# Kernel tuning notes

Measured on AMD Instinct MI355X. Metric: run time of the kernel, lower is better.

Reference implementation:

```python
import jax, jax.numpy as jnp
import numpy as np

P = 7          # output_size
SR = 2         # sampling_ratio
SCALES = (0.25, 0.125, 0.0625, 0.03125)
K_MIN, K_MAX = 2.0, 5.0   # -log2(max scale), -log2(min scale)
LVL0, S0, EPS = 4.0, 224.0, 1e-6  # torchvision LevelMapper defaults


def _coverage(x1, x2, size):
    """Fractional per-pixel coverage of interval [x1, x2] along an axis.
    Reproduces fill_masks_for_boxes edge weighting. x1, x2: [K] -> [K, size]."""
    cols = jnp.arange(size, dtype=x1.dtype)[None, :]
    x1f = jnp.floor(x1)[:, None]
    x2c = jnp.ceil(x2)[:, None]
    inside = ((cols >= x1f) & (cols < x2c)).astype(x1.dtype)
    wl = jnp.where(cols == x1f, 1.0 + x1f - x1[:, None], 1.0)
    wr = jnp.where(cols == x2c - 1.0, 1.0 + x2[:, None] - x2c, 1.0)
    return inside * wl * wr


def _axis_interp(coord, size):
    """torchvision roi_align (aligned=False) 1D bilinear setup.
    Returns lo/hi indices and weights (zeroed for out-of-range points)."""
    valid = ((coord >= -1.0) & (coord <= size)).astype(coord.dtype)
    c = jnp.maximum(coord, 0.0)
    lo0 = jnp.floor(c)
    top = lo0 >= size - 1
    lo = jnp.where(top, float(size - 1), lo0)
    hi = jnp.where(top, float(size - 1), lo0 + 1.0)
    c = jnp.where(top, float(size - 1), c)
    frac = c - lo
    return lo.astype(jnp.int32), hi.astype(jnp.int32), (1.0 - frac) * valid, frac * valid


def _level_roi(feat, scale, ub, bo, bidx):
    """Masked RoIAlign of the union box over one pyramid level.
    feat: [N,C,H,W]; ub, bo: [K,4] image-coord boxes; bidx: [K] int32."""
    N, C, H, W = feat.shape
    K = ub.shape[0]
    ubs = ub * scale
    bos = bo * scale

    def clipb(b):
        return (jnp.clip(b[:, 0], 0.0, W), jnp.clip(b[:, 1], 0.0, H),
                jnp.clip(b[:, 2], 0.0, W), jnp.clip(b[:, 3], 0.0, H))

    ux1, uy1, ux2, uy2 = clipb(ubs)
    ox1, oy1, ox2, oy2 = clipb(bos)
    # Separable pair-mask coverage (NOTE: torch code mutates boxes_h into the
    # union in-place before mask construction, so the 'h' mask is the union mask).
    cxu = _coverage(ux1, ux2, W)  # [K,W]
    cyu = _coverage(uy1, uy2, H)  # [K,H]
    cxo = _coverage(ox1, ox2, W)
    cyo = _coverage(oy1, oy2, H)

    x1, y1, x2, y2 = ubs[:, 0], ubs[:, 1], ubs[:, 2], ubs[:, 3]
    roi_w = jnp.maximum(x2 - x1, 1.0)
    roi_h = jnp.maximum(y2 - y1, 1.0)
    i = jnp.arange(P * SR)
    t = (i // SR).astype(jnp.float32) + ((i % SR).astype(jnp.float32) + 0.5) / SR  # bin units
    px = x1[:, None] + t[None, :] * (roi_w / P)[:, None]  # [K, P*SR]
    py = y1[:, None] + t[None, :] * (roi_h / P)[:, None]
    xlo, xhi, wxl, wxh = _axis_interp(px, W)
    ylo, yhi, wyl, wyh = _axis_interp(py, H)

    ga = lambda tab, idx: jnp.take_along_axis(tab, idx, axis=1)
    ys, wy = (ylo, yhi), (wyl, wyh)
    xs, wx = (xlo, xhi), (wxl, wxh)
    myu = (ga(cyu, ylo), ga(cyu, yhi))
    mxu = (ga(cxu, xlo), ga(cxu, xhi))
    myo = (ga(cyo, ylo), ga(cyo, yhi))
    mxo = (ga(cxo, xlo), ga(cxo, xhi))

    acc = jnp.zeros((K, P * SR, P * SR, C), dtype=feat.dtype)
    for a in range(2):
        for b in range(2):
            # gather corner features: [K, Ps, Ps, C]
            fv = feat[bidx[:, None, None], :, ys[a][:, :, None], xs[b][:, None, :]]
            m = jnp.maximum(myu[a][:, :, None] * mxu[b][:, None, :],
                            myo[a][:, :, None] * mxo[b][:, None, :])
            wgt = wy[a][:, :, None] * wx[b][:, None, :] * m
            acc = acc + wgt[..., None] * fv
    out = acc.reshape(K, P, SR, P, SR, C).mean(axis=(2, 4))  # avg over sample grid
    return jnp.transpose(out, (0, 3, 1, 2))  # [K, C, P, P]


def _forward(feat0, feat1, feat2, feat3, boxes_h, boxes_o):
    feats = (feat0, feat1, feat2, feat3)
    bidx = boxes_h[:, 0].astype(jnp.int32)
    bh = boxes_h[:, 1:]
    bo = boxes_o[:, 1:]
    ub = jnp.stack([jnp.minimum(bh[:, 0], bo[:, 0]), jnp.minimum(bh[:, 1], bo[:, 1]),
                    jnp.maximum(bh[:, 2], bo[:, 2]), jnp.maximum(bh[:, 3], bo[:, 3])], axis=1)
    # Level mapping (boxes_h already mutated into the union in the torch code)
    su = jnp.sqrt((ub[:, 2] - ub[:, 0]) * (ub[:, 3] - ub[:, 1]))
    so = jnp.sqrt((bo[:, 2] - bo[:, 0]) * (bo[:, 3] - bo[:, 1]))
    s = jnp.minimum(su, so)
    lv = (jnp.clip(jnp.floor(LVL0 + jnp.log2(s / S0 + EPS)), K_MIN, K_MAX)).astype(jnp.int32) - int(K_MIN)
    K, C = boxes_h.shape[0], feat0.shape[1]
    out = jnp.zeros((K, C, P, P), dtype=feat0.dtype)
    for l, (f, sc) in enumerate(zip(feats, SCALES)):
        ol = _level_roi(f, sc, ub, bo, bidx)
        out = out + jnp.where((lv == l)[:, None, None, None], ol, 0.0)
    return out


def setup_inputs() -> dict:
    key = jax.random.key(0)
    ks = jax.random.split(key, 12)
    feat0 = jax.random.normal(ks[0], (2, 256, 128, 128), dtype=jnp.float32)
    feat1 = jax.random.normal(ks[1], (2, 256, 64, 64), dtype=jnp.float32)
    feat2 = jax.random.normal(ks[2], (2, 256, 32, 32), dtype=jnp.float32)
    feat3 = jax.random.normal(ks[3], (2, 256, 16, 16), dtype=jnp.float32)
    K = 512
    bidx = jax.random.randint(ks[4], (K,), 0, 2).astype(jnp.float32)

    def mk(k):
        k1, k2, k3, k4 = jax.random.split(k, 4)
        x1 = jax.random.uniform(k1, (K,), minval=0.0, maxval=112.0)
        y1 = jax.random.uniform(k2, (K,), minval=0.0, maxval=112.0)
        w = jax.random.uniform(k3, (K,), minval=16.0, maxval=400.0)
        h = jax.random.uniform(k4, (K,), minval=16.0, maxval=400.0)
        return jnp.stack([bidx, x1, y1, x1 + w, y1 + h], axis=1)  # image is 512x512

    return {"feat0": feat0, "feat1": feat1, "feat2": feat2, "feat3": feat3,
            "boxes_h": mk(ks[5]), "boxes_o": mk(ks[6])}


def reference(feat0, feat1, feat2, feat3, boxes_h, boxes_o):
    return _forward(feat0, feat1, feat2, feat3, boxes_h, boxes_o)
```

## Files before the change

### kernel.cpp

```cpp
#include <hip/hip_runtime.h>
#include <math.h>

#define PP 7
#define CCH 256

__device__ __forceinline__ float coverage(float colf, float a, float b) {
    float af = floorf(a);
    float bc = ceilf(b);
    float v  = (colf >= af && colf < bc) ? 1.0f : 0.0f;
    float wl = (colf == af) ? (1.0f + af - a) : 1.0f;
    float wr = (colf == bc - 1.0f) ? (1.0f + b - bc) : 1.0f;
    return v * wl * wr;
}

__global__ __launch_bounds__(256) void nchw_to_nhwc(const float* __restrict__ src,
                                                    float* __restrict__ dst, int HW)
{
    __shared__ float tile[64][65];
    const int tx = threadIdx.x & 63, ty = threadIdx.x >> 6;
    const int pix0 = blockIdx.x * 64;
    const int c0   = blockIdx.y * 64;
    const int n    = blockIdx.z;

    const float* s = src + ((size_t)n * CCH + c0) * HW + pix0;
    #pragma unroll
    for (int i = 0; i < 16; ++i) {
        const int r = i*4 + ty;
        tile[r][tx] = s[(size_t)r * HW + tx];
    }
    __syncthreads();
    float* d = dst + ((size_t)n * HW + pix0) * CCH + c0;
    #pragma unroll
    for (int i = 0; i < 16; ++i) {
        const int p = i*4 + ty;
        d[(size_t)p * CCH + tx] = tile[tx][p];
    }
}

__global__ __launch_bounds__(256) void roi_gather_nhwc(
    const float* __restrict__ n0, const float* __restrict__ n1,
    const float* __restrict__ n2, const float* __restrict__ n3,
    const float* __restrict__ bh, const float* __restrict__ bo,
    float* __restrict__ out, int K)
{
    const int k  = blockIdx.x;
    const int py = blockIdx.y;
    const int c  = threadIdx.x;

    __shared__ int   t_xoff_lo[14], t_xoff_hi[14];
    __shared__ float t_wxl[14], t_wxh[14];
    __shared__ float t_cxu0[14], t_cxu1[14], t_cxo0[14], t_cxo1[14];
    __shared__ int   s_yoff_lo[2], s_yoff_hi[2];
    __shared__ float s_wyl[2], s_wyh[2];
    __shared__ float s_cyu0[2], s_cyu1[2], s_cyo0[2], s_cyo1[2];

    const float hx1 = bh[k*5+1], hy1 = bh[k*5+2], hx2 = bh[k*5+3], hy2 = bh[k*5+4];
    const float px1 = bo[k*5+1], py1 = bo[k*5+2], px2 = bo[k*5+3], py2 = bo[k*5+4];
    const int   bimg = (int)bh[k*5+0];

    const float ux1 = fminf(hx1, px1), uy1 = fminf(hy1, py1);
    const float ux2 = fmaxf(hx2, px2), uy2 = fmaxf(hy2, py2);
    const float su = sqrtf((ux2-ux1)*(uy2-uy1));
    const float so = sqrtf((px2-px1)*(py2-py1));
    const float s  = fminf(su, so);
    float lvf = floorf(4.0f + log2f(s/224.0f + 1e-6f));
    lvf = fminf(fmaxf(lvf, 2.0f), 5.0f);
    const int lv = (int)lvf - 2;

    const float scales[4] = {0.25f, 0.125f, 0.0625f, 0.03125f};
    const int   dims[4]   = {128, 64, 32, 16};
    const float scale = scales[lv];
    const int   W = dims[lv], H = W;
    const int   HW = W * H;
    const float Wf = (float)W, Hf = (float)H;
    const float* nh = (lv == 0) ? n0 : (lv == 1) ? n1 : (lv == 2) ? n2 : n3;

    const float usx1 = ux1*scale, usy1 = uy1*scale, usx2 = ux2*scale, usy2 = uy2*scale;
    const float osx1 = px1*scale, osy1 = py1*scale, osx2 = px2*scale, osy2 = py2*scale;
    const float cux1 = fminf(fmaxf(usx1, 0.f), Wf), cux2 = fminf(fmaxf(usx2, 0.f), Wf);
    const float cuy1 = fminf(fmaxf(usy1, 0.f), Hf), cuy2 = fminf(fmaxf(usy2, 0.f), Hf);
    const float cox1 = fminf(fmaxf(osx1, 0.f), Wf), cox2 = fminf(fmaxf(osx2, 0.f), Wf);
    const float coy1 = fminf(fmaxf(osy1, 0.f), Hf), coy2 = fminf(fmaxf(osy2, 0.f), Hf);
    const float roi_w = fmaxf(usx2 - usx1, 1.0f);
    const float roi_h = fmaxf(usy2 - usy1, 1.0f);

    if (threadIdx.x < 14) {
        const int i = threadIdx.x;
        const float t = (float)(i >> 1) + 0.25f + 0.5f*(float)(i & 1);
        const float p = usx1 + t * (roi_w / 7.0f);
        const float valid = (p >= -1.0f && p <= Wf) ? 1.0f : 0.0f;
        float cc = fmaxf(p, 0.0f);
        const float lo0 = floorf(cc);
        const bool top = (lo0 >= Wf - 1.0f);
        const float lo = top ? (Wf - 1.0f) : lo0;
        const float hi = top ? (Wf - 1.0f) : (lo0 + 1.0f);
        cc = top ? (Wf - 1.0f) : cc;
        const float frac = cc - lo;
        t_xoff_lo[i] = (int)lo * CCH;  t_xoff_hi[i] = (int)hi * CCH;
        t_wxl[i] = (1.0f - frac) * valid;  t_wxh[i] = frac * valid;
        t_cxu0[i] = coverage(lo, cux1, cux2);
        t_cxu1[i] = coverage(hi, cux1, cux2);
        t_cxo0[i] = coverage(lo, cox1, cox2);
        t_cxo1[i] = coverage(hi, cox1, cox2);
    } else if (threadIdx.x >= 64 && threadIdx.x < 66) {
        const int isy = threadIdx.x - 64;
        const int i = 2*py + isy;
        const float t = (float)(i >> 1) + 0.25f + 0.5f*(float)(i & 1);
        const float p = usy1 + t * (roi_h / 7.0f);
        const float valid = (p >= -1.0f && p <= Hf) ? 1.0f : 0.0f;
        float cc = fmaxf(p, 0.0f);
        const float lo0 = floorf(cc);
        const bool top = (lo0 >= Hf - 1.0f);
        const float lo = top ? (Hf - 1.0f) : lo0;
        const float hi = top ? (Hf - 1.0f) : (lo0 + 1.0f);
        cc = top ? (Hf - 1.0f) : cc;
        const float frac = cc - lo;
        s_yoff_lo[isy] = (int)lo * W * CCH;  s_yoff_hi[isy] = (int)hi * W * CCH;
        s_wyl[isy] = (1.0f - frac) * valid;  s_wyh[isy] = frac * valid;
        s_cyu0[isy] = coverage(lo, cuy1, cuy2);
        s_cyu1[isy] = coverage(hi, cuy1, cuy2);
        s_cyo0[isy] = coverage(lo, coy1, coy2);
        s_cyo1[isy] = coverage(hi, coy1, coy2);
    }
    __syncthreads();

    const float* pb = nh + (size_t)bimg * HW * CCH + c;

    float accs[7] = {0,0,0,0,0,0,0};

    #pragma unroll
    for (int isy = 0; isy < 2; ++isy) {
        const int   yoL = s_yoff_lo[isy], yoH = s_yoff_hi[isy];
        const float wyl = s_wyl[isy], wyh = s_wyh[isy];
        const float cyu0 = s_cyu0[isy], cyu1 = s_cyu1[isy];
        const float cyo0 = s_cyo0[isy], cyo1 = s_cyo1[isy];
        #pragma unroll
        for (int ix = 0; ix < 14; ++ix) {
            const int pxb = ix >> 1;
            const int xoL = t_xoff_lo[ix], xoH = t_xoff_hi[ix];
            const float wxl = t_wxl[ix], wxh = t_wxh[ix];
            const float cxu0 = t_cxu0[ix], cxu1 = t_cxu1[ix];
            const float cxo0 = t_cxo0[ix], cxo1 = t_cxo1[ix];
            const float w00 = wyl*wxl*fmaxf(cyu0*cxu0, cyo0*cxo0);
            const float w01 = wyl*wxh*fmaxf(cyu0*cxu1, cyo0*cxo1);
            const float w10 = wyh*wxl*fmaxf(cyu1*cxu0, cyo1*cxo0);
            const float w11 = wyh*wxh*fmaxf(cyu1*cxu1, cyo1*cxo1);
            const float a00 = pb[yoL + xoL], a01 = pb[yoL + xoH];
            const float a10 = pb[yoH + xoL], a11 = pb[yoH + xoH];
            accs[pxb] += w00*a00 + w01*a01 + w10*a10 + w11*a11;
        }
    }

    float* op = out + ((size_t)k * CCH + c) * (PP * PP) + py * PP;
    #pragma unroll
    for (int pxb = 0; pxb < 7; ++pxb) op[pxb] = accs[pxb] * 0.25f;
}

__global__ __launch_bounds__(256) void roi_pair_kernel(
    const float* __restrict__ f0, const float* __restrict__ f1,
    const float* __restrict__ f2, const float* __restrict__ f3,
    const float* __restrict__ bh, const float* __restrict__ bo,
    float* __restrict__ out, int K)
{
    const int k  = blockIdx.x;
    const int py = blockIdx.y;
    const int c  = threadIdx.x;

    __shared__ int   t_xlo[14], t_xhi[14];
    __shared__ float t_wxl[14], t_wxh[14], t_cxu0[14], t_cxu1[14], t_cxo0[14], t_cxo1[14];
    __shared__ int   s_ylo[2], s_yhi[2];
    __shared__ float s_wyl[2], s_wyh[2], s_cyu0[2], s_cyu1[2], s_cyo0[2], s_cyo1[2];

    const float hx1 = bh[k*5+1], hy1 = bh[k*5+2], hx2 = bh[k*5+3], hy2 = bh[k*5+4];
    const float px1 = bo[k*5+1], py1 = bo[k*5+2], px2 = bo[k*5+3], py2 = bo[k*5+4];
    const int   bimg = (int)bh[k*5+0];

    const float ux1 = fminf(hx1, px1), uy1 = fminf(hy1, py1);
    const float ux2 = fmaxf(hx2, px2), uy2 = fmaxf(hy2, py2);
    const float su = sqrtf((ux2-ux1)*(uy2-uy1));
    const float so = sqrtf((px2-px1)*(py2-py1));
    const float s  = fminf(su, so);
    float lvf = floorf(4.0f + log2f(s/224.0f + 1e-6f));
    lvf = fminf(fmaxf(lvf, 2.0f), 5.0f);
    const int lv = (int)lvf - 2;

    const float scales[4] = {0.25f, 0.125f, 0.0625f, 0.03125f};
    const int   dims[4]   = {128, 64, 32, 16};
    const float scale = scales[lv];
    const int   W = dims[lv], H = W;
    const float Wf = (float)W, Hf = (float)H;
    const float* feat = (lv == 0) ? f0 : (lv == 1) ? f1 : (lv == 2) ? f2 : f3;

    const float usx1 = ux1*scale, usy1 = uy1*scale, usx2 = ux2*scale, usy2 = uy2*scale;
    const float osx1 = px1*scale, osy1 = py1*scale, osx2 = px2*scale, osy2 = py2*scale;
    const float cux1 = fminf(fmaxf(usx1, 0.f), Wf), cux2 = fminf(fmaxf(usx2, 0.f), Wf);
    const float cuy1 = fminf(fmaxf(usy1, 0.f), Hf), cuy2 = fminf(fmaxf(usy2, 0.f), Hf);
    const float cox1 = fminf(fmaxf(osx1, 0.f), Wf), cox2 = fminf(fmaxf(osx2, 0.f), Wf);
    const float coy1 = fminf(fmaxf(osy1, 0.f), Hf), coy2 = fminf(fmaxf(osy2, 0.f), Hf);
    const float roi_w = fmaxf(usx2 - usx1, 1.0f);
    const float roi_h = fmaxf(usy2 - usy1, 1.0f);

    if (threadIdx.x < 14) {
        const int i = threadIdx.x;
        const float t = (float)(i >> 1) + 0.25f + 0.5f*(float)(i & 1);
        const float p = usx1 + t * (roi_w / 7.0f);
        const float valid = (p >= -1.0f && p <= Wf) ? 1.0f : 0.0f;
        float cc = fmaxf(p, 0.0f);
        const float lo0 = floorf(cc);
        const bool top = (lo0 >= Wf - 1.0f);
        const float lo = top ? (Wf - 1.0f) : lo0;
        const float hi = top ? (Wf - 1.0f) : (lo0 + 1.0f);
        cc = top ? (Wf - 1.0f) : cc;
        const float frac = cc - lo;
        t_xlo[i] = (int)lo;  t_xhi[i] = (int)hi;
        t_wxl[i] = (1.0f - frac) * valid;  t_wxh[i] = frac * valid;
        t_cxu0[i] = coverage(lo, cux1, cux2);
        t_cxu1[i] = coverage(hi, cux1, cux2);
        t_cxo0[i] = coverage(lo, cox1, cox2);
        t_cxo1[i] = coverage(hi, cox1, cox2);
    } else if (threadIdx.x >= 64 && threadIdx.x < 66) {
        const int isy = threadIdx.x - 64;
        const int i = 2*py + isy;
        const float t = (float)(i >> 1) + 0.25f + 0.5f*(float)(i & 1);
        const float p = usy1 + t * (roi_h / 7.0f);
        const float valid = (p >= -1.0f && p <= Hf) ? 1.0f : 0.0f;
        float cc = fmaxf(p, 0.0f);
        const float lo0 = floorf(cc);
        const bool top = (lo0 >= Hf - 1.0f);
        const float lo = top ? (Hf - 1.0f) : lo0;
        const float hi = top ? (Hf - 1.0f) : (lo0 + 1.0f);
        cc = top ? (Hf - 1.0f) : cc;
        const float frac = cc - lo;
        s_ylo[isy] = (int)lo;  s_yhi[isy] = (int)hi;
        s_wyl[isy] = (1.0f - frac) * valid;  s_wyh[isy] = frac * valid;
        s_cyu0[isy] = coverage(lo, cuy1, cuy2);
        s_cyu1[isy] = coverage(hi, cuy1, cuy2);
        s_cyo0[isy] = coverage(lo, coy1, coy2);
        s_cyo1[isy] = coverage(hi, coy1, coy2);
    }
    __syncthreads();

    const float* fc = feat + (size_t)(bimg * CCH + c) * (H * W);
    float accs[7] = {0,0,0,0,0,0,0};

    #pragma unroll
    for (int isy = 0; isy < 2; ++isy) {
        const int   ylo = s_ylo[isy], yhi = s_yhi[isy];
        const float wyl = s_wyl[isy], wyh = s_wyh[isy];
        const float cyu0 = s_cyu0[isy], cyu1 = s_cyu1[isy];
        const float cyo0 = s_cyo0[isy], cyo1 = s_cyo1[isy];
        const float* rlo = fc + ylo * W;
        const float* rhi = fc + yhi * W;
        #pragma unroll
        for (int ix = 0; ix < 14; ++ix) {
            const int pxb = ix >> 1;
            const int xlo = t_xlo[ix], xhi = t_xhi[ix];
            const float wxl = t_wxl[ix], wxh = t_wxh[ix];
            const float cxu0 = t_cxu0[ix], cxu1 = t_cxu1[ix];
            const float cxo0 = t_cxo0[ix], cxo1 = t_cxo1[ix];
            const float w00 = wyl*wxl*fmaxf(cyu0*cxu0, cyo0*cxo0);
            const float w01 = wyl*wxh*fmaxf(cyu0*cxu1, cyo0*cxo1);
            const float w10 = wyh*wxl*fmaxf(cyu1*cxu0, cyo1*cxo0);
            const float w11 = wyh*wxh*fmaxf(cyu1*cxu1, cyo1*cxo1);
            accs[pxb] += w00*rlo[xlo] + w01*rlo[xhi] + w10*rhi[xlo] + w11*rhi[xhi];
        }
    }

    float* op = out + ((size_t)k * CCH + c) * (PP * PP) + py * PP;
    #pragma unroll
    for (int pxb = 0; pxb < 7; ++pxb) op[pxb] = accs[pxb] * 0.25f;
}

extern "C" void kernel_launch(void* const* d_in, const int* in_sizes, int n_in,
                              void* d_out, int out_size, void* d_ws, size_t ws_size,
                              hipStream_t stream) {
    const float* f0 = (const float*)d_in[0];
    const float* f1 = (const float*)d_in[1];
    const float* f2 = (const float*)d_in[2];
    const float* f3 = (const float*)d_in[3];
    const float* bh = (const float*)d_in[4];
    const float* bo = (const float*)d_in[5];
    float* out = (float*)d_out;
    const int K = in_sizes[4] / 5;
    const int NIMG = in_sizes[0] / (CCH * 128 * 128);

    const size_t hw0 = 128*128, hw1 = 64*64, hw2 = 32*32, hw3 = 16*16;
    const size_t sz0 = (size_t)NIMG * CCH * hw0;
    const size_t sz1 = (size_t)NIMG * CCH * hw1;
    const size_t sz2 = (size_t)NIMG * CCH * hw2;
    const size_t sz3 = (size_t)NIMG * CCH * hw3;
    const size_t need_bytes = (sz0 + sz1 + sz2 + sz3) * sizeof(float);

    if (ws_size >= need_bytes) {
        float* w0 = (float*)d_ws;
        float* w1 = w0 + sz0;
        float* w2 = w1 + sz1;
        float* w3 = w2 + sz2;

        nchw_to_nhwc<<<dim3((int)(hw0/64), 4, NIMG), 256, 0, stream>>>(f0, w0, (int)hw0);
        nchw_to_nhwc<<<dim3((int)(hw1/64), 4, NIMG), 256, 0, stream>>>(f1, w1, (int)hw1);
        nchw_to_nhwc<<<dim3((int)(hw2/64), 4, NIMG), 256, 0, stream>>>(f2, w2, (int)hw2);
        nchw_to_nhwc<<<dim3((int)(hw3/64), 4, NIMG), 256, 0, stream>>>(f3, w3, (int)hw3);

        roi_gather_nhwc<<<dim3(K, PP), CCH, 0, stream>>>(w0, w1, w2, w3, bh, bo, out, K);
    } else {
        roi_pair_kernel<<<dim3(K, PP), CCH, 0, stream>>>(f0, f1, f2, f3, bh, bo, out, K);
    }
}
```

Before: 146.5 us.

## Merge transpose launches and restructure RoI gather to precompute bin weights

The four per-level NCHW-to-NHWC transpose launches become a single launch that decodes level, image, channel block and pixel tile from a flat block index, removing three launch gaps. The gather kernel now runs one block per RoI and channel half (128 threads) and loops over all 7 output rows, instead of one block per RoI and output row. Bilinear-times-mask weights for all 49 bins are precomputed once into shared memory and read back as float4, which removes the redundant per-row setup and per-thread weight arithmetic. The cost is fewer, longer blocks (1024 instead of 3584), so there is less parallelism to hide gather latency, and each thread now does a serial loop over rows.

```diff
diff --git a/kernel.cpp b/kernel.cpp
--- a/kernel.cpp
+++ b/kernel.cpp
@@ -13,20 +13,33 @@
     return v * wl * wr;
 }
 
-__global__ __launch_bounds__(256) void nchw_to_nhwc(const float* __restrict__ src,
-                                                    float* __restrict__ dst, int HW)
+__global__ __launch_bounds__(256) void nchw_to_nhwc_all(
+    const float* __restrict__ f0, const float* __restrict__ f1,
+    const float* __restrict__ f2, const float* __restrict__ f3,
+    float* __restrict__ w0, float* __restrict__ w1,
+    float* __restrict__ w2, float* __restrict__ w3, int NIMG)
 {
     __shared__ float tile[64][65];
+    int b = blockIdx.x;
+    const float* src; float* dst; int HW, hw64;
+    const int t0 = NIMG * 1024, t1 = t0 + NIMG * 256, t2 = t1 + NIMG * 64;
+    if (b < t0)      {          src = f0; dst = w0; HW = 16384; hw64 = 256; }
+    else if (b < t1) { b -= t0; src = f1; dst = w1; HW = 4096;  hw64 = 64;  }
+    else if (b < t2) { b -= t1; src = f2; dst = w2; HW = 1024;  hw64 = 16;  }
+    else             { b -= t2; src = f3; dst = w3; HW = 256;   hw64 = 4;   }
+    const int tpi  = hw64 * 4;
+    const int n    = b / tpi;
+    const int r    = b - n * tpi;
+    const int cb   = r / hw64;
+    const int pix0 = (r - cb * hw64) * 64;
+    const int c0   = cb * 64;
+
     const int tx = threadIdx.x & 63, ty = threadIdx.x >> 6;
-    const int pix0 = blockIdx.x * 64;
-    const int c0   = blockIdx.y * 64;
-    const int n    = blockIdx.z;
-
     const float* s = src + ((size_t)n * CCH + c0) * HW + pix0;
     #pragma unroll
     for (int i = 0; i < 16; ++i) {
-        const int r = i*4 + ty;
-        tile[r][tx] = s[(size_t)r * HW + tx];
+        const int rr = i*4 + ty;
+        tile[rr][tx] = s[(size_t)rr * HW + tx];
     }
     __syncthreads();
     float* d = dst + ((size_t)n * HW + pix0) * CCH + c0;
@@ -37,22 +50,22 @@
     }
 }
 
-__global__ __launch_bounds__(256) void roi_gather_nhwc(
+__global__ __launch_bounds__(128) void roi_gather_nhwc(
     const float* __restrict__ n0, const float* __restrict__ n1,
     const float* __restrict__ n2, const float* __restrict__ n3,
     const float* __restrict__ bh, const float* __restrict__ bo,
     float* __restrict__ out, int K)
 {
-    const int k  = blockIdx.x;
-    const int py = blockIdx.y;
-    const int c  = threadIdx.x;
+    const int k    = blockIdx.x;
+    const int half = blockIdx.y;
+    const int tid  = threadIdx.x;
+    const int c    = half * 128 + tid;
 
     __shared__ int   t_xoff_lo[14], t_xoff_hi[14];
-    __shared__ float t_wxl[14], t_wxh[14];
-    __shared__ float t_cxu0[14], t_cxu1[14], t_cxo0[14], t_cxo1[14];
-    __shared__ int   s_yoff_lo[2], s_yoff_hi[2];
-    __shared__ float s_wyl[2], s_wyh[2];
-    __shared__ float s_cyu0[2], s_cyu1[2], s_cyo0[2], s_cyo1[2];
+    __shared__ int   s_yoff_lo[14], s_yoff_hi[14];
+    __shared__ float wbin[49][16];
+    __shared__ float t_wxl[14], t_wxh[14], t_cxu0[14], t_cxu1[14], t_cxo0[14], t_cxo1[14];
+    __shared__ float t_wyl[14], t_wyh[14], t_cyu0[14], t_cyu1[14], t_cyo0[14], t_cyo1[14];
 
     const float hx1 = bh[k*5+1], hy1 = bh[k*5+2], hx2 = bh[k*5+3], hy2 = bh[k*5+4];
     const float px1 = bo[k*5+1], py1 = bo[k*5+2], px2 = bo[k*5+3], py2 = bo[k*5+4];
@@ -84,8 +97,8 @@
     const float roi_w = fmaxf(usx2 - usx1, 1.0f);
     const float roi_h = fmaxf(usy2 - usy1, 1.0f);
 
-    if (threadIdx.x < 14) {
-        const int i = threadIdx.x;
+    if (tid < 14) {
+        const int i = tid;
         const float t = (float)(i >> 1) + 0.25f + 0.5f*(float)(i & 1);
         const float p = usx1 + t * (roi_w / 7.0f);
         const float valid = (p >= -1.0f && p <= Wf) ? 1.0f : 0.0f;
@@ -102,9 +115,8 @@
         t_cxu1[i] = coverage(hi, cux1, cux2);
         t_cxo0[i] = coverage(lo, cox1, cox2);
         t_cxo1[i] = coverage(hi, cox1, cox2);
-    } else if (threadIdx.x >= 64 && threadIdx.x < 66) {
-        const int isy = threadIdx.x - 64;
-        const int i = 2*py + isy;
+    } else if (tid >= 64 && tid < 78) {
+        const int i = tid - 64;
         const float t = (float)(i >> 1) + 0.25f + 0.5f*(float)(i & 1);
         const float p = usy1 + t * (roi_h / 7.0f);
         const float valid = (p >= -1.0f && p <= Hf) ? 1.0f : 0.0f;
@@ -115,45 +127,61 @@
         const float hi = top ? (Hf - 1.0f) : (lo0 + 1.0f);
         cc = top ? (Hf - 1.0f) : cc;
         const float frac = cc - lo;
-        s_yoff_lo[isy] = (int)lo * W * CCH;  s_yoff_hi[isy] = (int)hi * W * CCH;
-        s_wyl[isy] = (1.0f - frac) * valid;  s_wyh[isy] = frac * valid;
-        s_cyu0[isy] = coverage(lo, cuy1, cuy2);
-        s_cyu1[isy] = coverage(hi, cuy1, cuy2);
-        s_cyo0[isy] = coverage(lo, coy1, coy2);
-        s_cyo1[isy] = coverage(hi, coy1, coy2);
+        s_yoff_lo[i] = (int)lo * W * CCH;  s_yoff_hi[i] = (int)hi * W * CCH;
+        t_wyl[i] = (1.0f - frac) * valid;  t_wyh[i] = frac * valid;
+        t_cyu0[i] = coverage(lo, cuy1, cuy2);
+        t_cyu1[i] = coverage(hi, cuy1, cuy2);
+        t_cyo0[i] = coverage(lo, coy1, coy2);
+        t_cyo1[i] = coverage(hi, coy1, coy2);
     }
     __syncthreads();
 
+    if (tid < 49) {
+        const int bpy = tid / 7, bpx = tid - bpy * 7;
+        #pragma unroll
+        for (int isy = 0; isy < 2; ++isy) {
+            const int sy = 2*bpy + isy;
+            const float wy0 = t_wyl[sy], wy1 = t_wyh[sy];
+            const float yu0 = t_cyu0[sy], yu1 = t_cyu1[sy];
+            const float yo0 = t_cyo0[sy], yo1 = t_cyo1[sy];
+            #pragma unroll
+            for (int isx = 0; isx < 2; ++isx) {
+                const int sxm = 2*bpx + isx;
+                const float wx0 = t_wxl[sxm], wx1 = t_wxh[sxm];
+                const float xu0 = t_cxu0[sxm], xu1 = t_cxu1[sxm];
+                const float xo0 = t_cxo0[sxm], xo1 = t_cxo1[sxm];
+                const int p4 = (isy*2 + isx) * 4;
+                wbin[tid][p4+0] = wy0*wx0*fmaxf(yu0*xu0, yo0*xo0);
+                wbin[tid][p4+1] = wy0*wx1*fmaxf(yu0*xu1, yo0*xo1);
+                wbin[tid][p4+2] = wy1*wx0*fmaxf(yu1*xu0, yo1*xo0);
+                wbin[tid][p4+3] = wy1*wx1*fmaxf(yu1*xu1, yo1*xo1);
+            }
+        }
+    }
+    __syncthreads();
+
     const float* pb = nh + (size_t)bimg * HW * CCH + c;
-
-    float accs[7] = {0,0,0,0,0,0,0};
-
-    #pragma unroll
-    for (int isy = 0; isy < 2; ++isy) {
-        const int   yoL = s_yoff_lo[isy], yoH = s_yoff_hi[isy];
-        const float wyl = s_wyl[isy], wyh = s_wyh[isy];
-        const float cyu0 = s_cyu0[isy], cyu1 = s_cyu1[isy];
-        const float cyo0 = s_cyo0[isy], cyo1 = s_cyo1[isy];
+    float* okc = out + (size_t)k * (CCH * PP * PP) + (size_t)c * (PP * PP);
+
+    for (int pyy = 0; pyy < 7; ++pyy) {
+        float accs[7] = {0,0,0,0,0,0,0};
         #pragma unroll
-        for (int ix = 0; ix < 14; ++ix) {
-            const int pxb = ix >> 1;
-            const int xoL = t_xoff_lo[ix], xoH = t_xoff_hi[ix];
-            const float wxl = t_wxl[ix], wxh = t_wxh[ix];
-            const float cxu0 = t_cxu0[ix], cxu1 = t_cxu1[ix];
-            const float cxo0 = t_cxo0[ix], cxo1 = t_cxo1[ix];
-            const float w00 = wyl*wxl*fmaxf(cyu0*cxu0, cyo0*cxo0);
-            const float w01 = wyl*wxh*fmaxf(cyu0*cxu1, cyo0*cxo1);
-            const float w10 = wyh*wxl*fmaxf(cyu1*cxu0, cyo1*cxo0);
-            const float w11 = wyh*wxh*fmaxf(cyu1*cxu1, cyo1*cxo1);
-            const float a00 = pb[yoL + xoL], a01 = pb[yoL + xoH];
-            const float a10 = pb[yoH + xoL], a11 = pb[yoH + xoH];
-            accs[pxb] += w00*a00 + w01*a01 + w10*a10 + w11*a11;
+        for (int isy = 0; isy < 2; ++isy) {
+            const int sy  = 2*pyy + isy;
+            const int yoL = s_yoff_lo[sy], yoH = s_yoff_hi[sy];
+            #pragma unroll
+            for (int ix = 0; ix < 14; ++ix) {
+                const int pxb = ix >> 1, isx = ix & 1;
+                const float4 w = *(const float4*)&wbin[pyy*7 + pxb][(isy*2 + isx)*4];
+                const int xoL = t_xoff_lo[ix], xoH = t_xoff_hi[ix];
+                accs[pxb] += w.x*pb[yoL + xoL] + w.y*pb[yoL + xoH]
+                           + w.z*pb[yoH + xoL] + w.w*pb[yoH + xoH];
+            }
         }
-    }
-
-    float* op = out + ((size_t)k * CCH + c) * (PP * PP) + py * PP;
-    #pragma unroll
-    for (int pxb = 0; pxb < 7; ++pxb) op[pxb] = accs[pxb] * 0.25f;
+        float* op = okc + pyy * PP;
+        #pragma unroll
+        for (int q = 0; q < 7; ++q) op[q] = accs[q] * 0.25f;
+    }
 }
 
 __global__ __launch_bounds__(256) void roi_pair_kernel(
@@ -297,12 +325,9 @@
         float* w2 = w1 + sz1;
         float* w3 = w2 + sz2;
 
-        nchw_to_nhwc<<<dim3((int)(hw0/64), 4, NIMG), 256, 0, stream>>>(f0, w0, (int)hw0);
-        nchw_to_nhwc<<<dim3((int)(hw1/64), 4, NIMG), 256, 0, stream>>>(f1, w1, (int)hw1);
-        nchw_to_nhwc<<<dim3((int)(hw2/64), 4, NIMG), 256, 0, stream>>>(f2, w2, (int)hw2);
-        nchw_to_nhwc<<<dim3((int)(hw3/64), 4, NIMG), 256, 0, stream>>>(f3, w3, (int)hw3);
-
-        roi_gather_nhwc<<<dim3(K, PP), CCH, 0, stream>>>(w0, w1, w2, w3, bh, bo, out, K);
+        const int tiles = NIMG * (1024 + 256 + 64 + 16);
+        nchw_to_nhwc_all<<<tiles, 256, 0, stream>>>(f0, f1, f2, f3, w0, w1, w2, w3, NIMG);
+        roi_gather_nhwc<<<dim3(K, 2), 128, 0, stream>>>(w0, w1, w2, w3, bh, bo, out, K);
     } else {
         roi_pair_kernel<<<dim3(K, PP), CCH, 0, stream>>>(f0, f1, f2, f3, bh, bo, out, K);
     }
```

Result: no change. 146.6 us (+0.1%).
